# Optimization experiments

Hardware: AMD Instinct MI355X
Metric: run time of the kernel (lower is better)

The kernel has to match this reference:

```python
import jax, jax.numpy as jnp
import numpy as np

N_CLS = 5  # number of modalities / graph nodes


def _l2norm(x, eps=1e-12):
    n = jnp.linalg.norm(x, axis=-1, keepdims=True)
    return x / jnp.maximum(n, eps)


def _bn(x, g, b, eps=1e-5):
    """BatchNorm over channel axis 1 (training-mode batch stats), x: (B, Ch, ...)."""
    axes = (0,) + tuple(range(2, x.ndim))
    m = x.mean(axis=axes, keepdims=True)
    v = x.var(axis=axes, keepdims=True)
    shp = (1, -1) + (1,) * (x.ndim - 2)
    return g.reshape(shp) * (x - m) / jnp.sqrt(v + eps) + b.reshape(shp)


def _cross_attn(y, x, wq, wk, wv):
    """ME-GraphAU-style CrossAttn over the spatial (hw) axis. y,x: (..., hw, c)."""
    q = y @ wq  # (..., hw, c/2)
    k = x @ wk
    v = x @ wv
    scale = 1.0 / jnp.sqrt(jnp.asarray(wq.shape[1], jnp.float32))
    attn = jax.nn.softmax(jnp.einsum('...qd,...kd->...qk', q, k) * scale, axis=-1)
    return jnp.einsum('...qk,...kd->...qd', attn, v)


def _gnn_layer(x, edge, U, V, A, Bm, E, bnv_g, bnv_b, bne_g, bne_b, mask_node):
    """One edge-vertex GNN update. x: (b,n,t,c), edge: (b,n*n,t,c).
    Edge e = i*n + j has end-node i, start-node j (create_e_matrix layout)."""
    b, n, t, c = x.shape
    idx_i = jnp.repeat(jnp.arange(n), n)  # 'end' one-hot gather
    idx_j = jnp.tile(jnp.arange(n), n)    # 'start' one-hot gather
    res = x
    Vix = x @ A
    Vjx = x @ Bm
    e = edge @ E
    edge1 = Vix[:, idx_i] + Vjx[:, idx_j] + e  # einsum('ev,bvtc->betc') as gather
    edge1 = _bn(edge1, bne_g, bne_b)
    edge1 = jnp.where(jnp.isnan(edge1), 0.0, edge1)
    edge = edge + jax.nn.relu(edge1)
    eg = jax.nn.sigmoid(edge).reshape(b, n, n, t, c)
    eg = jax.nn.softmax(eg, axis=2).reshape(b, n * n, t, c)  # softmax over start nodes j
    Ujx = (x @ V)[:, idx_j]
    # einsum('ve,betc->bvtc', end.T, e*Ujx): scatter-sum edges to their end node i
    agg = (eg * Ujx).reshape(b, n, n, t, c).sum(axis=2) / n
    xn = x @ U + agg
    x1 = _bn(xn, bnv_g, bnv_b)
    if mask_node:
        x1 = jnp.where(jnp.isnan(x1), 0.0, x1)
    x = jax.nn.relu(res + x1)
    return x, edge


def _forward(af, ef, gf, attf, sf,
             fam_q, fam_k, fam_v, arm_q, arm_k, arm_v,
             edge_proj_w, edge_proj_b, gem_bn_g, gem_bn_b,
             U1, V1, A1, B1, E1, U2, V2, A2, B2, E2,
             bnv1_g, bnv1_b, bne1_g, bne1_b, bnv2_g, bnv2_b, bne2_g, bne2_b,
             sc, edge_fc_w, edge_fc_b):
    b, c, t, h, w = af.shape
    hw = h * w
    n = N_CLS

    def prep(f):  # (b,c,t,h,w) -> (b,t,hw,c)
        return f.reshape(b, c, t, hw).transpose(0, 2, 3, 1)

    mods = [prep(f) for f in (af, ef, gf, attf, sf)]
    f_u = jnp.stack(mods, axis=1)           # (b, 5, t, hw, c)
    f_v = f_u.mean(axis=-2)                 # (b, 5, t, c)

    # --- GEM edge extractor (ME-GraphAU style, adapted to the extra t axis) ---
    gfeat = jnp.broadcast_to(mods[0][:, None], f_u.shape)  # global feature = af
    feat = _cross_attn(f_u, gfeat, fam_q, fam_k, fam_v)    # FAM
    idx_i = jnp.repeat(jnp.arange(n), n)
    idx_j = jnp.tile(jnp.arange(n), n)
    feat_end = feat[:, idx_i]               # (b, 25, t, hw, c)
    feat_start = feat[:, idx_j]
    feat = _cross_attn(feat_start, feat_end, arm_q, arm_k, arm_v)  # ARM
    edge = feat @ edge_proj_w + edge_proj_b
    edge = _bn(edge.reshape(b, n * n, t * hw, c), gem_bn_g, gem_bn_b)
    f_e = edge.reshape(b, n * n, t, hw, c).mean(axis=-2)   # (b, 25, t, c)

    # --- 2-layer edge-vertex GNN ---
    f_v, f_e = _gnn_layer(f_v, f_e, U1, V1, A1, B1, E1,
                          bnv1_g, bnv1_b, bne1_g, bne1_b, mask_node=True)
    f_v, f_e = _gnn_layer(f_v, f_e, U2, V2, A2, B2, E2,
                          bnv2_g, bnv2_b, bne2_g, bne2_b, mask_node=False)

    # --- cosine-similarity head ---
    scn = _l2norm(jax.nn.relu(sc))                         # (5, c)
    cl = (_l2norm(f_v) * scn[None, :, None, :]).sum(axis=-1)  # (b, 5, t)
    cl_edge = jnp.einsum('bntc,c->bnt', f_e, edge_fc_w)[..., None] + edge_fc_b  # (b,25,t,1)
    return cl, cl_edge


def setup_inputs() -> dict:
    B, C, T, H, W = 8, 256, 16, 7, 7
    key = jax.random.key(0)
    ks = jax.random.split(key, 40)
    d = {}
    for i, name in enumerate(['af', 'ef', 'gf', 'attf', 'sf']):
        d[name] = jax.random.normal(ks[i], (B, C, T, H, W), jnp.float32)
    gs = float(np.sqrt(2.0 / C))   # GNN linear init scale
    xs = float(np.sqrt(2.0 / (2 * C)))  # xavier-like
    k = 5
    def nrm(shape, s):
        nonlocal k
        k += 1
        return jax.random.normal(ks[k], shape, jnp.float32) * s
    d['fam_q'] = nrm((C, C // 2), xs); d['fam_k'] = nrm((C, C // 2), xs); d['fam_v'] = nrm((C, C), xs)
    d['arm_q'] = nrm((C, C // 2), xs); d['arm_k'] = nrm((C, C // 2), xs); d['arm_v'] = nrm((C, C), xs)
    d['edge_proj_w'] = nrm((C, C), xs); d['edge_proj_b'] = jnp.zeros((C,), jnp.float32)
    d['gem_bn_g'] = jnp.ones((N_CLS * N_CLS,), jnp.float32); d['gem_bn_b'] = jnp.zeros((N_CLS * N_CLS,), jnp.float32)
    for nm in ['U1', 'V1', 'A1', 'B1', 'E1', 'U2', 'V2', 'A2', 'B2', 'E2']:
        d[nm] = nrm((C, C), gs)
    for nm, sz in [('bnv1', N_CLS), ('bne1', N_CLS * N_CLS), ('bnv2', N_CLS), ('bne2', N_CLS * N_CLS)]:
        d[nm + '_g'] = jnp.ones((sz,), jnp.float32)
        d[nm + '_b'] = jnp.zeros((sz,), jnp.float32)
    d['sc'] = nrm((N_CLS, C), xs)
    d['edge_fc_w'] = nrm((C,), xs)
    d['edge_fc_b'] = jnp.zeros((1,), jnp.float32)
    return d


def reference(af, ef, gf, attf, sf,
              fam_q, fam_k, fam_v, arm_q, arm_k, arm_v,
              edge_proj_w, edge_proj_b, gem_bn_g, gem_bn_b,
              U1, V1, A1, B1, E1, U2, V2, A2, B2, E2,
              bnv1_g, bnv1_b, bne1_g, bne1_b, bnv2_g, bnv2_b, bne2_g, bne2_b,
              sc, edge_fc_w, edge_fc_b):
    return _forward(af, ef, gf, attf, sf,
                    fam_q, fam_k, fam_v, arm_q, arm_k, arm_v,
                    edge_proj_w, edge_proj_b, gem_bn_g, gem_bn_b,
                    U1, V1, A1, B1, E1, U2, V2, A2, B2, E2,
                    bnv1_g, bnv1_b, bne1_g, bne1_b, bnv2_g, bnv2_b, bne2_g, bne2_b,
                    sc, edge_fc_w, edge_fc_b)
```

## Files before the change

### kernel.cpp

```cpp
#include <hip/hip_runtime.h>

#define DEV __device__ __forceinline__

typedef unsigned short bhalf;
typedef __attribute__((ext_vector_type(8))) short bf8v;
typedef __attribute__((ext_vector_type(4))) float f4;
typedef __attribute__((ext_vector_type(4))) unsigned short us4;

namespace {
constexpr int TPB = 256;
constexpr float ATT_SCALE = 0.08838834764831845f;

constexpr size_t O_PT  = 0;
constexpr size_t O_WTS = 20971520;
constexpr size_t O_K1B = 21626880;
constexpr size_t O_FW  = 23724032;
constexpr size_t O_VQT = 27918336;
constexpr size_t O_VKT = 30015488;
constexpr size_t O_G   = 32112640;
constexpr size_t O_VWT = 36306944;
constexpr size_t O_Q2B = 40501248;
constexpr size_t O_K2B = 50987008;
constexpr size_t O_W2T = 61472768;
constexpr size_t O_FV  = 82444288;
constexpr size_t O_HWS = 83099648;
constexpr size_t O_EDG = 86376448;
constexpr size_t O_XA  = 89654272;
constexpr size_t O_XB  = 90309632;
constexpr size_t O_XU  = 90964992;
constexpr size_t O_XV  = 91620352;
constexpr size_t O_EE  = 92275712;
constexpr size_t O_ET  = 95552512;
constexpr size_t O_XN  = 98829312;
constexpr size_t O_GWT = 99484672;
constexpr size_t O_CSE = 100795392;
constexpr size_t O_FVB = 100796416;
constexpr size_t O_HWB = 101124096;
constexpr size_t O_EDB = 102762496;

constexpr size_t W_FAMQ = 0, W_FAMK = 32768, W_ARMQ = 65536, W_ARMK = 98304,
                 W_FAMV = 131072, W_ARMV = 196608, W_EPW = 262144;
constexpr size_t FW_VQ = 0, FW_VK = 32768, FW_VW = 65536;

constexpr int ST_GS1 = 0, ST_GS2 = 256;
}


DEV bhalf f2b(float f) {
  unsigned u = __float_as_uint(f);
  return (bhalf)((u + 0x7FFFu + ((u >> 16) & 1u)) >> 16);
}

DEV f4 mfma16(bf8v a, bf8v b, f4 c) {
  return __builtin_amdgcn_mfma_f32_16x16x32_bf16(a, b, c, 0, 0, 0);
}

DEV bf8v ldfrag(const bhalf* base, int r0, int k0, int S, int l) {
  return *reinterpret_cast<const bf8v*>(base + (size_t)(r0 + (l & 15)) * S + k0 + ((l >> 4) << 3));
}

DEV bf8v ldswz(const bhalf* base, int row, int koffB, int strideB) {
  int byte = row * strideB + koffB;
  byte ^= ((row & 7) << 4);
  return *reinterpret_cast<const bf8v*>(reinterpret_cast<const char*>(base) + byte);
}

DEV float sumShards(const float* base, int idx) {
  float s = 0.f;
  #pragma unroll
  for (int x = 0; x < 8; ++x) s += base[x*32 + idx];
  return s;
}

DEV void regSoftmax(float sv[4][4]) {
  #pragma unroll
  for (int reg = 0; reg < 4; ++reg) {
    float m = fmaxf(fmaxf(sv[0][reg], sv[1][reg]), fmaxf(sv[2][reg], sv[3][reg]));
    #pragma unroll
    for (int off = 1; off <= 8; off <<= 1) m = fmaxf(m, __shfl_xor(m, off));
    float s = 0.f;
    #pragma unroll
    for (int nt = 0; nt < 4; ++nt) { float e = __expf(sv[nt][reg] - m); sv[nt][reg] = e; s += e; }
    #pragma unroll
    for (int off = 1; off <= 8; off <<= 1) s += __shfl_xor(s, off);
    float inv = 1.f / s;
    #pragma unroll
    for (int nt = 0; nt < 4; ++nt) sv[nt][reg] *= inv;
  }
}

DEV void reduce2Atomic(float a, float b, float* ga, float* gb, float* red) {
  #pragma unroll
  for (int off = 32; off; off >>= 1) { a += __shfl_down(a, off); b += __shfl_down(b, off); }
  if ((threadIdx.x & 63) == 0) { int w = threadIdx.x >> 6; red[w*2] = a; red[w*2+1] = b; }
  __syncthreads();
  if (threadIdx.x == 0) {
    atomicAdd(ga, red[0]+red[2]+red[4]+red[6]);
    atomicAdd(gb, red[1]+red[3]+red[5]+red[7]);
  }
  __syncthreads();
}


__global__ void __launch_bounds__(256) prepAll(const float* fq, const float* fk, const float* fv,
                                               const float* aq, const float* ak, const float* av,
                                               const float* ep, bhalf* WT,
                                               const float* af, const float* ef, const float* gf,
                                               const float* attf, const float* sf,
                                               bhalf* PT, float* FV, float* G,
                                               const float* A1, const float* B1, const float* U1,
                                               const float* V1, const float* E1,
                                               const float* A2, const float* B2, const float* U2,
                                               const float* V2, const float* E2,
                                               bhalf* GWT, float* CSE, bhalf* FVB) {
  __shared__ float lb[49*260];
  int tid = threadIdx.x;
  if (blockIdx.x < 1280) {
    int blk = blockIdx.x;
    const float* src; bhalf* dst; int N, n;
    if (blk < 512) {
      int m = blk >> 7; n = blk & 127; N = 128;
      src = (m==0)?fq:(m==1)?fk:(m==2)?aq:ak;
      dst = WT + (size_t)m*32768;
    } else {
      int r = blk - 512; int m = r >> 8; n = r & 255; N = 256;
      src = (m==0)?fv:(m==1)?av:ep;
      dst = WT + 131072 + (size_t)m*65536;
    }
    dst[(size_t)n*256 + tid] = f2b(src[(size_t)tid*N + n]);
  } else if (blockIdx.x < 1920) {
    int blk = blockIdx.x - 1280;
    int u = blk % 5, bt = blk / 5, b = bt >> 4, t = bt & 15;
    const float* src = (u==0)?af:(u==1)?ef:(u==2)?gf:(u==3)?attf:sf;
    src += ((size_t)b*256*16 + t)*49;
    for (int o = tid; o < 49*256; o += TPB) {
      int c = o / 49, p = o % 49;
      lb[p*260 + c] = src[(size_t)c*784 + p];
    }
    __syncthreads();
    bhalf* pt = PT + (size_t)blk*16384;
    for (int p = 0; p < 64; ++p)
      pt[p*256 + tid] = (p < 49) ? f2b(lb[p*260 + tid]) : (bhalf)0;
    float s = 0.f;
    for (int p = 0; p < 49; ++p) s += lb[p*260 + tid];
    float mval = s * (1.f/49.f);
    size_t idx = (((size_t)(b*5+u)*16) + t)*256 + tid;
    FV[idx] = mval;
    FVB[idx] = f2b(mval);
  } else if (blockIdx.x < 2176) {
    int c = blockIdx.x - 1920;
    const float* ar = av + (size_t)c*256;
    float acc = 0.f;
    for (int d = 0; d < 256; ++d)
      acc = fmaf(ar[d], ep[(size_t)d*256 + tid], acc);
    G[(size_t)c*256 + tid] = acc;
  } else if (blockIdx.x < 4736) {
    int blk = blockIdx.x - 2176;
    int m = blk >> 8, n = blk & 255;
    const float* src = (m==0)?A1:(m==1)?B1:(m==2)?U1:(m==3)?V1:(m==4)?E1:
                       (m==5)?A2:(m==6)?B2:(m==7)?U2:(m==8)?V2:E2;
    GWT[(size_t)m*65536 + (size_t)n*256 + tid] = f2b(src[(size_t)tid*256 + n]);
  } else {
    float s = 0.f;
    for (int c = 0; c < 256; ++c) s += E1[(size_t)c*256 + tid];
    CSE[tid] = s;
  }
}

__global__ void __launch_bounds__(256) wf2(const float* fv, const float* aq, const float* ak,
                                           const float* G, bhalf* FW) {
  int blk = blockIdx.x, tid = threadIdx.x;
  if (blk < 256) {
    int k = blk;
    if (tid < 128) {
      float a1 = 0.f, a2 = 0.f;
      for (int c = 0; c < 256; ++c) {
        float f = fv[(size_t)k*256 + c];
        a1 = fmaf(f, aq[(size_t)c*128 + tid], a1);
        a2 = fmaf(f, ak[(size_t)c*128 + tid], a2);
      }
      FW[FW_VQ + (size_t)tid*256 + k] = f2b(a1);
      FW[FW_VK + (size_t)tid*256 + k] = f2b(a2);
    }
  } else {
    int k = blk - 256;
    float a = 0.f;
    for (int c = 0; c < 256; ++c)
      a = fmaf(fv[(size_t)k*256 + c], G[(size_t)c*256 + tid], a);
    FW[FW_VW + (size_t)tid*256 + k] = f2b(a);
  }
}

__global__ void __launch_bounds__(256, 4) kv1(const bhalf* PT, const bhalf* WT, const bhalf* FW,
                                              bhalf* K1B, bhalf* VQT, bhalf* VKT, bhalf* VWT,
                                              bhalf* Q2B) {
  __shared__ bhalf Wl[64*256];
  int bt = blockIdx.x, part = blockIdx.y;
  int tid = threadIdx.x, w = tid >> 6, l = tid & 63;
  const bhalf* Wsrc; int nt0;
  const bhalf* A;
  if (part >= 10) {
    int u = (part - 10) >> 1;
    nt0 = ((part - 10) & 1) * 4;
    Wsrc = WT + W_FAMQ;
    A = PT + (size_t)(bt*5 + u)*16384;
  } else if (part < 2) {
    nt0 = part*4; Wsrc = WT + W_FAMK; A = PT + (size_t)bt*5*16384;
  } else if (part < 6) {
    nt0 = ((part - 2) & 1) * 4;
    Wsrc = FW + (((part - 2) >> 1) == 0 ? FW_VQ : FW_VK);
    A = PT + (size_t)bt*5*16384;
  } else {
    nt0 = (part - 6)*4; Wsrc = FW + FW_VW; A = PT + (size_t)bt*5*16384;
  }
  bf8v a8[8];
  #pragma unroll
  for (int kt = 0; kt < 8; ++kt) a8[kt] = ldfrag(A, w*16, kt*32, 256, l);
  {
    const char* gw = reinterpret_cast<const char*>(Wsrc + (size_t)nt0*16*256);
    char* lw = reinterpret_cast<char*>(Wl);
    #pragma unroll
    for (int c = 0; c < 8; ++c) {
      int x = (c*256 + tid) << 4;
      float4 val = *reinterpret_cast<const float4*>(gw + x);
      *reinterpret_cast<float4*>(lw + (x ^ (((x >> 9) & 7) << 4))) = val;
    }
  }
  __syncthreads();
  __builtin_amdgcn_s_setprio(1);
  f4 accs[4];
  #pragma unroll
  for (int nn = 0; nn < 4; ++nn) {
    f4 acc = {0.f,0.f,0.f,0.f};
    #pragma unroll
    for (int kt = 0; kt < 8; ++kt)
      acc = mfma16(a8[kt], ldswz(Wl, nn*16 + (l & 15), kt*64 + ((l >> 4) << 4), 512), acc);
    accs[nn] = acc;
  }
  __builtin_amdgcn_s_setprio(0);
  if (part >= 10) {
    int u = (part - 10) >> 1;
    bhalf* q1 = Q2B + (size_t)(bt*5 + u)*8192;
    #pragma unroll
    for (int nn = 0; nn < 4; ++nn) {
      int nt = nt0 + nn;
      #pragma unroll
      for (int reg = 0; reg < 4; ++reg) {
        int p = w*16 + ((l>>4)<<2) + reg;
        q1[(size_t)p*128 + nt*16 + (l&15)] = f2b(accs[nn][reg]);
      }
    }
  } else if (part < 2) {
    bhalf* dst = K1B + (size_t)bt*8192;
    #pragma unroll
    for (int nn = 0; nn < 4; ++nn) {
      int nt = nt0 + nn;
      #pragma unroll
      for (int reg = 0; reg < 4; ++reg) {
        int p = w*16 + ((l>>4)<<2) + reg;
        dst[(size_t)p*128 + nt*16 + (l&15)] = f2b(accs[nn][reg]);
      }
    }
  } else if (part < 6) {
    bhalf* o = ((((part - 2) >> 1) == 0) ? VQT : VKT) + (size_t)bt*8192;
    #pragma unroll
    for (int nn = 0; nn < 4; ++nn) {
      int n = (nt0 + nn)*16 + (l&15);
      int p0 = w*16 + ((l>>4)<<2);
      us4 pk = { f2b(accs[nn][0]), f2b(accs[nn][1]), f2b(accs[nn][2]), f2b(accs[nn][3]) };
      *reinterpret_cast<us4*>(o + (size_t)n*64 + p0) = pk;
    }
  } else {
    bhalf* ow = VWT + (size_t)bt*16384;
    #pragma unroll
    for (int nn = 0; nn < 4; ++nn) {
      int n = (nt0 + nn)*16 + (l&15);
      int p0 = w*16 + ((l>>4)<<2);
      us4 pk = { f2b(accs[nn][0]), f2b(accs[nn][1]), f2b(accs[nn][2]), f2b(accs[nn][3]) };
      *reinterpret_cast<us4*>(ow + (size_t)n*64 + p0) = pk;
    }
  }
}

__global__ void __launch_bounds__(256) s1ker(const bhalf* WT,
    const bhalf* K1B, const bhalf* VQT, const bhalf* VKT, const bhalf* VWT,
    bhalf* Q2B, bhalf* K2B, bhalf* W2T)
{
  __shared__ bhalf bufP[64*72];
  int orig = blockIdx.x;
  int blk = (orig & 7) * 80 + (orig >> 3);
  int bt = blk / 5;
  int tid = threadIdx.x, w = tid >> 6, l = tid & 63;
  float sv[4][4];
  {
    const bhalf* Q1 = Q2B + (size_t)blk*8192;
    const bhalf* K1 = K1B + (size_t)bt*8192;
    bf8v aq[4];
    #pragma unroll
    for (int kt = 0; kt < 4; ++kt) aq[kt] = ldfrag(Q1, w*16, kt*32, 128, l);
    __builtin_amdgcn_s_setprio(1);
    #pragma unroll
    for (int nt = 0; nt < 4; ++nt) {
      f4 acc = {0.f,0.f,0.f,0.f};
      #pragma unroll
      for (int kt = 0; kt < 4; ++kt)
        acc = mfma16(aq[kt], ldfrag(K1, nt*16, kt*32, 128, l), acc);
      #pragma unroll
      for (int reg = 0; reg < 4; ++reg) sv[nt][reg] = acc[reg] * ATT_SCALE;
    }
    __builtin_amdgcn_s_setprio(0);
  }
  if ((l & 15) > 0) { sv[3][0] = -1e30f; sv[3][1] = -1e30f; sv[3][2] = -1e30f; sv[3][3] = -1e30f; }
  regSoftmax(sv);
  #pragma unroll
  for (int nt = 0; nt < 4; ++nt)
    #pragma unroll
    for (int reg = 0; reg < 4; ++reg)
      bufP[(w*16 + ((l>>4)<<2) + reg)*72 + nt*16 + (l&15)] = f2b(sv[nt][reg]);
  __syncthreads();
  bf8v ap0[4], ap1[4];
  #pragma unroll
  for (int g = 0; g < 4; ++g) {
    ap0[g] = ldfrag(bufP, g*16, 0, 72, l);
    ap1[g] = ldfrag(bufP, g*16, 32, 72, l);
  }
  const bhalf* vq = VQT + (size_t)bt*8192;
  const bhalf* vk = VKT + (size_t)bt*8192;
  const bhalf* vw = VWT + (size_t)bt*16384;
  bhalf* q2 = Q2B + (size_t)blk*8192;
  bhalf* k2 = K2B + (size_t)blk*8192;
  bhalf* w2 = W2T + (size_t)blk*16384;
  __builtin_amdgcn_s_setprio(1);
  #pragma unroll
  for (int nn = 0; nn < 2; ++nn) {
    int nt = w*2 + nn;
    bf8v b0 = ldfrag(vq, nt*16, 0, 64, l);
    bf8v b1 = ldfrag(vq, nt*16, 32, 64, l);
    f4 acc[4];
    #pragma unroll
    for (int g = 0; g < 4; ++g) {
      f4 z = {0.f,0.f,0.f,0.f};
      z = mfma16(ap0[g], b0, z);
      acc[g] = mfma16(ap1[g], b1, z);
    }
    int c = nt*16 + (l & 15);
    #pragma unroll
    for (int g = 0; g < 4; ++g)
      #pragma unroll
      for (int reg = 0; reg < 4; ++reg) {
        int p = g*16 + ((l>>4)<<2) + reg;
        q2[(size_t)p*128 + c] = (p < 49) ? f2b(acc[g][reg]) : (bhalf)0;
      }
  }
  #pragma unroll
  for (int nn = 0; nn < 2; ++nn) {
    int nt = w*2 + nn;
    bf8v b0 = ldfrag(vk, nt*16, 0, 64, l);
    bf8v b1 = ldfrag(vk, nt*16, 32, 64, l);
    f4 acc[4];
    #pragma unroll
    for (int g = 0; g < 4; ++g) {
      f4 z = {0.f,0.f,0.f,0.f};
      z = mfma16(ap0[g], b0, z);
      acc[g] = mfma16(ap1[g], b1, z);
    }
    int c = nt*16 + (l & 15);
    #pragma unroll
    for (int g = 0; g < 4; ++g)
      #pragma unroll
      for (int reg = 0; reg < 4; ++reg) {
        int p = g*16 + ((l>>4)<<2) + reg;
        k2[(size_t)p*128 + c] = (p < 49) ? f2b(acc[g][reg]) : (bhalf)0;
      }
  }
  #pragma unroll
  for (int nn = 0; nn < 4; ++nn) {
    int nt = w*4 + nn;
    bf8v b0 = ldfrag(vw, nt*16, 0, 64, l);
    bf8v b1 = ldfrag(vw, nt*16, 32, 64, l);
    f4 acc[4];
    #pragma unroll
    for (int g = 0; g < 4; ++g) {
      f4 z = {0.f,0.f,0.f,0.f};
      z = mfma16(ap0[g], b0, z);
      acc[g] = mfma16(ap1[g], b1, z);
    }
    int c = nt*16 + (l & 15);
    int p0 = (l >> 4) << 2;
    #pragma unroll
    for (int g = 0; g < 4; ++g) {
      int pb = g*16 + p0;
      us4 pk = { (bhalf)((pb+0 < 49) ? f2b(acc[g][0]) : 0),
                 (bhalf)((pb+1 < 49) ? f2b(acc[g][1]) : 0),
                 (bhalf)((pb+2 < 49) ? f2b(acc[g][2]) : 0),
                 (bhalf)((pb+3 < 49) ? f2b(acc[g][3]) : 0) };
      *reinterpret_cast<us4*>(w2 + (size_t)c*64 + pb) = pk;
    }
  }
  __builtin_amdgcn_s_setprio(0);
}

__global__ void __launch_bounds__(256) s2ker(const bhalf* Q2B, const bhalf* K2B, const bhalf* W2T,
    const float* epb, float* hws, bhalf* hwsb, float* gs1, float* gs2)
{
  __shared__ bhalf Kl[64*128];
  __shared__ bhalf bufP[64*72];
  __shared__ float redH[256];
  __shared__ float redS[8];
  int orig = blockIdx.x;
  int blk = (orig & 7) * 400 + (orig >> 3);
  int e = blk % 25, bt = blk / 25, b = bt >> 4, t = bt & 15;
  int i = e / 5, j = e % 5;
  int tid = threadIdx.x, w = tid >> 6, l = tid & 63;
  const bhalf* K = K2B + (size_t)(bt*5 + i)*8192;
  const bhalf* V = W2T + (size_t)(bt*5 + i)*16384;
  const bhalf* Q = Q2B + (size_t)(bt*5 + j)*8192;
  bf8v aq[4];
  #pragma unroll
  for (int kt = 0; kt < 4; ++kt) aq[kt] = ldfrag(Q, w*16, kt*32, 128, l);
  {
    const char* gk = reinterpret_cast<const char*>(K);
    char* lk = reinterpret_cast<char*>(Kl);
    #pragma unroll
    for (int c = 0; c < 4; ++c) {
      int x = (c*256 + tid) << 4;
      float4 val = *reinterpret_cast<const float4*>(gk + x);
      *reinterpret_cast<float4*>(lk + (x ^ (((x >> 8) & 7) << 4))) = val;
    }
  }
  __syncthreads();
  float sv[4][4];
  __builtin_amdgcn_s_setprio(1);
  #pragma unroll
  for (int nt = 0; nt < 4; ++nt) {
    f4 acc = {0.f,0.f,0.f,0.f};
    #pragma unroll
    for (int kt = 0; kt < 4; ++kt)
      acc = mfma16(aq[kt], ldswz(Kl, nt*16 + (l & 15), kt*64 + ((l >> 4) << 4), 256), acc);
    #pragma unroll
    for (int reg = 0; reg < 4; ++reg) sv[nt][reg] = acc[reg] * ATT_SCALE;
  }
  __builtin_amdgcn_s_setprio(0);
  if ((l & 15) > 0) { sv[3][0] = -1e30f; sv[3][1] = -1e30f; sv[3][2] = -1e30f; sv[3][3] = -1e30f; }
  regSoftmax(sv);
  #pragma unroll
  for (int nt = 0; nt < 4; ++nt)
    #pragma unroll
    for (int reg = 0; reg < 4; ++reg)
      bufP[(w*16 + ((l>>4)<<2) + reg)*72 + nt*16 + (l&15)] = f2b(sv[nt][reg]);
  bf8v vf0[4], vf1[4];
  #pragma unroll
  for (int nn = 0; nn < 4; ++nn) {
    vf0[nn] = ldfrag(V, (w*4 + nn)*16, 0, 64, l);
    vf1[nn] = ldfrag(V, (w*4 + nn)*16, 32, 64, l);
  }
  __syncthreads();
  bf8v ap0[4], ap1[4];
  #pragma unroll
  for (int g = 0; g < 4; ++g) {
    ap0[g] = ldfrag(bufP, g*16, 0, 72, l);
    ap1[g] = ldfrag(bufP, g*16, 32, 72, l);
  }
  float sqa = 0.f;
  __builtin_amdgcn_s_setprio(1);
  #pragma unroll
  for (int nn = 0; nn < 4; ++nn) {
    f4 acc[4];
    #pragma unroll
    for (int g = 0; g < 4; ++g) {
      f4 z = {0.f,0.f,0.f,0.f};
      z = mfma16(ap0[g], vf0[nn], z);
      acc[g] = mfma16(ap1[g], vf1[nn], z);
    }
    int c = ((w*4 + nn) << 4) + (l & 15);
    float bias = epb[c];
    float hw = 0.f;
    #pragma unroll
    for (int g = 0; g < 4; ++g) {
      #pragma unroll
      for (int reg = 0; reg < 4; ++reg) {
        int p = g*16 + ((l>>4)<<2) + reg;
        if (p < 49) { float v = acc[g][reg] + bias; hw += v; sqa += v*v; }
      }
    }
    hw += __shfl_xor(hw, 16);
    hw += __shfl_xor(hw, 32);
    if ((l >> 4) == 0) redH[c] = hw;
  }
  __builtin_amdgcn_s_setprio(0);
  __syncthreads();
  float hwtot = redH[tid];
  size_t oidx = (((size_t)(b*25+e)*16) + t)*256 + tid;
  hws[oidx] = hwtot;
  hwsb[oidx] = f2b(hwtot);
  int slot = (orig & 7)*32 + e;
  reduce2Atomic(hwtot, sqa, gs1 + slot, gs2 + slot, redS);
}


__global__ void __launch_bounds__(256, 2) gnnProjN(const bhalf* Xb, const bhalf* GW,
    float* xA, float* xB, float* xU, float* xV) {
  __shared__ bhalf Wl[64*256];
  int blk = blockIdx.x;
  int tid = threadIdx.x, w = tid >> 6, l = tid & 63;
  int m = blk / 40, rem = blk % 40, rt = rem >> 2, ct = rem & 3;
  const bhalf* A = Xb + (size_t)rt*64*256;
  const bhalf* Wsrc = GW + (size_t)m*65536;
  float* dst = (m==0)?xA:(m==1)?xB:(m==2)?xU:xV;
  bf8v a8[8];
  #pragma unroll
  for (int kt = 0; kt < 8; ++kt) a8[kt] = ldfrag(A, w*16, kt*32, 256, l);
  {
    const char* gw = reinterpret_cast<const char*>(Wsrc + (size_t)ct*64*256);
    char* lw = reinterpret_cast<char*>(Wl);
    #pragma unroll
    for (int c = 0; c < 8; ++c) {
      int x = (c*256 + tid) << 4;
      float4 val = *reinterpret_cast<const float4*>(gw + x);
      *reinterpret_cast<float4*>(lw + (x ^ (((x >> 9) & 7) << 4))) = val;
    }
  }
  __syncthreads();
  __builtin_amdgcn_s_setprio(1);
  f4 accs[4];
  #pragma unroll
  for (int nn = 0; nn < 4; ++nn) {
    f4 acc = {0.f,0.f,0.f,0.f};
    #pragma unroll
    for (int kt = 0; kt < 8; ++kt)
      acc = mfma16(a8[kt], ldswz(Wl, nn*16 + (l & 15), kt*64 + ((l >> 4) << 4), 512), acc);
    accs[nn] = acc;
  }
  __builtin_amdgcn_s_setprio(0);
  int p0 = w*16 + ((l>>4)<<2);
  size_t rbase = (size_t)rt*64 + p0;
  #pragma unroll
  for (int nn = 0; nn < 4; ++nn) {
    int n = ct*64 + nn*16 + (l&15);
    #pragma unroll
    for (int reg = 0; reg < 4; ++reg)
      dst[(rbase + reg)*256 + n] = accs[nn][reg];
  }
}

__global__ void __launch_bounds__(256, 2) gnnProjE(const bhalf* Eb, const bhalf* GW,
    const float* CSE, const float* gs1, const float* gs2, const float* gg, const float* gb,
    int bnfly, const float* xA, const float* xB, float* ET, float* es1, float* es2) {
  __shared__ bhalf Wl[64*256];
  int blk = blockIdx.x;
  int tid = threadIdx.x, w = tid >> 6, l = tid & 63;
  int rt = blk >> 2, ct = blk & 3;
  const bhalf* A = Eb + (size_t)rt*64*256;
  bf8v a8[8];
  #pragma unroll
  for (int kt = 0; kt < 8; ++kt) a8[kt] = ldfrag(A, w*16, kt*32, 256, l);
  {
    const char* gw = reinterpret_cast<const char*>(GW + (size_t)ct*64*256);
    char* lw = reinterpret_cast<char*>(Wl);
    #pragma unroll
    for (int c = 0; c < 8; ++c) {
      int x = (c*256 + tid) << 4;
      float4 val = *reinterpret_cast<const float4*>(gw + x);
      *reinterpret_cast<float4*>(lw + (x ^ (((x >> 9) & 7) << 4))) = val;
    }
  }
  __syncthreads();
  __builtin_amdgcn_s_setprio(1);
  f4 accs[4];
  #pragma unroll
  for (int nn = 0; nn < 4; ++nn) {
    f4 acc = {0.f,0.f,0.f,0.f};
    #pragma unroll
    for (int kt = 0; kt < 8; ++kt)
      acc = mfma16(a8[kt], ldswz(Wl, nn*16 + (l & 15), kt*64 + ((l >> 4) << 4), 512), acc);
    accs[nn] = acc;
  }
  __builtin_amdgcn_s_setprio(0);
  int be = rt*4 + w;
  int b = be / 25, e = be % 25;
  int i = e / 5, j = e % 5;
  const float* xAr = xA + ((size_t)(b*5+i)*16)*256;
  const float* xBr = xB + ((size_t)(b*5+j)*16)*256;
  float scl = 1.f, ofs = 0.f;
  if (bnfly) {
    constexpr float invCnt = 1.f/1605632.f;
    float m = sumShards(gs1, e)*invCnt;
    float var = sumShards(gs2, e)*invCnt - m*m;
    float rstd = rsqrtf(var + 1e-5f);
    float g = gg[e]*rstd;
    scl = g * (1.f/49.f);
    ofs = gb[e] - g*m;
  }
  int t0 = (l>>4)<<2;
  float s1l = 0.f, s2l = 0.f;
  #pragma unroll
  for (int nn = 0; nn < 4; ++nn) {
    int n = ct*64 + nn*16 + (l&15);
    float cs = CSE[n] * ofs;
    #pragma unroll
    for (int reg = 0; reg < 4; ++reg) {
      int t = t0 + reg;
      float ve = fmaf(accs[nn][reg], scl, cs);
      float vfull = xAr[(size_t)t*256 + n] + xBr[(size_t)t*256 + n] + ve;
      ET[((size_t)be*16 + t)*256 + n] = vfull;
      s1l += vfull; s2l += vfull*vfull;
    }
  }
  #pragma unroll
  for (int off = 32; off; off >>= 1) { s1l += __shfl_down(s1l, off); s2l += __shfl_down(s2l, off); }
  if (l == 0) {
    int slot = (blk & 7)*32 + e;
    atomicAdd(es1 + slot, s1l);
    atomicAdd(es2 + slot, s2l);
  }
}

__global__ void __launch_bounds__(256) g2bg3a(const float* ET, const float* HWS, const float* EDGin,
    float* EDGout, bhalf* EDGb, const float* xV, const float* xU, float* XN,
    const float* gs1, const float* gs2, const float* gemg, const float* gemb,
    const float* bg, const float* bb2, const float* es1, const float* es2,
    float* ns1, float* ns2, const float* efw, const float* efb, float* out, int layer) {
  __shared__ float red[8];
  int blk = blockIdx.x, tid = threadIdx.x;
  int b = blk / 80, i = (blk >> 4) % 5, t = blk & 15;
  constexpr float inv32k = 1.f/32768.f;
  constexpr float invCnt = 1.f/1605632.f;
  float ssum = 0.f, exv[5], xvv[5];
  #pragma unroll
  for (int j = 0; j < 5; ++j) {
    int e = i*5 + j;
    size_t ee = ((size_t)(b*25 + e)*16 + t)*256 + tid;
    float m = sumShards(es1, e)*inv32k;
    float var = sumShards(es2, e)*inv32k - m*m;
    float rstd = rsqrtf(var + 1e-5f);
    float v = bg[e]*((ET[ee]-m)*rstd) + bb2[e];
    if (v != v) v = 0.f;
    float base;
    if (layer == 0) {
      float gm = sumShards(gs1, e)*invCnt;
      float gvar = sumShards(gs2, e)*invCnt - gm*gm;
      float gr = rsqrtf(gvar + 1e-5f);
      base = gemg[e]*((HWS[ee]*(1.f/49.f) - gm)*gr) + gemb[e];
    } else {
      base = EDGin[ee];
    }
    float edg = base + fmaxf(v, 0.f);
    if (layer == 0) {
      EDGout[ee] = edg;
      EDGb[ee] = f2b(edg);
    } else {
      float vv = edg * efw[tid];
      #pragma unroll
      for (int off = 32; off; off >>= 1) vv += __shfl_down(vv, off);
      if ((tid & 63) == 0) red[tid >> 6] = vv;
      __syncthreads();
      if (tid == 0) out[640 + (size_t)(b*25 + e)*16 + t] = red[0]+red[1]+red[2]+red[3] + efb[0];
      __syncthreads();
    }
    float sg = 1.f/(1.f + __expf(-edg));
    exv[j] = __expf(sg);
    ssum += exv[j];
    xvv[j] = xV[((size_t)(b*5+j)*16 + t)*256 + tid];
  }
  float agg = 0.f;
  #pragma unroll
  for (int j = 0; j < 5; ++j) agg += exv[j]*xvv[j];
  agg *= 0.2f/ssum;
  float xn = xU[(size_t)blk*256 + tid] + agg;
  XN[(size_t)blk*256 + tid] = xn;
  int slot = (blk & 7)*32 + i;
  reduce2Atomic(xn, xn*xn, ns1 + slot, ns2 + slot, red);
}

__global__ void __launch_bounds__(256) g3b(const float* XN, float* X, bhalf* Xb,
                                           const float* g, const float* bb,
                                           const float* s1, const float* s2, int mask) {
  int blk = blockIdx.x, tid = threadIdx.x;
  int i = (blk >> 4) % 5;
  size_t ni = (size_t)blk*256 + tid;
  constexpr float invCnt = 1.f/32768.f;
  float m = sumShards(s1, i)*invCnt;
  float var = sumShards(s2, i)*invCnt - m*m;
  float rstd = rsqrtf(var + 1e-5f);
  float v = g[i]*((XN[ni]-m)*rstd) + bb[i];
  if (mask && v != v) v = 0.f;
  float nv = fmaxf(X[ni] + v, 0.f);
  X[ni] = nv;
  Xb[ni] = f2b(nv);
}

__global__ void __launch_bounds__(256) g3bfin(const float* XN, const float* FV,
    const float* g, const float* bb, const float* s1, const float* s2,
    const float* sc, float* out) {
  __shared__ float red[12];
  int blk = blockIdx.x, tid = threadIdx.x;
  int i = (blk >> 4) % 5;
  size_t ni = (size_t)blk*256 + tid;
  constexpr float inv32k = 1.f/32768.f;
  float m = sumShards(s1, i)*inv32k;
  float var = sumShards(s2, i)*inv32k - m*m;
  float rstd = rsqrtf(var + 1e-5f);
  float v = g[i]*((XN[ni]-m)*rstd) + bb[i];
  float x = fmaxf(FV[ni] + v, 0.f);
  float s = fmaxf(sc[i*256 + tid], 0.f);
  float xx = x*x, ss = s*s, xs = x*s;
  #pragma unroll
  for (int off = 32; off; off >>= 1) {
    xx += __shfl_down(xx, off); ss += __shfl_down(ss, off); xs += __shfl_down(xs, off);
  }
  if ((tid & 63) == 0) { int w = tid >> 6; red[w*3] = xx; red[w*3+1] = ss; red[w*3+2] = xs; }
  __syncthreads();
  if (tid == 0) {
    float sxx = red[0]+red[3]+red[6]+red[9];
    float sss = red[1]+red[4]+red[7]+red[10];
    float sxs = red[2]+red[5]+red[8]+red[11];
    float nx = fmaxf(sqrtf(sxx), 1e-12f);
    float ns = fmaxf(sqrtf(sss), 1e-12f);
    out[blk] = sxs / (nx * ns);
  }
}


extern "C" void kernel_launch(void* const* d_in, const int* in_sizes, int n_in,
                              void* d_out, int out_size, void* d_ws, size_t ws_size,
                              hipStream_t stream) {
  (void)in_sizes; (void)n_in; (void)out_size; (void)ws_size;
  const float* af    = (const float*)d_in[0];
  const float* ef    = (const float*)d_in[1];
  const float* gfm   = (const float*)d_in[2];
  const float* attf  = (const float*)d_in[3];
  const float* sfm   = (const float*)d_in[4];
  const float* fam_q = (const float*)d_in[5];
  const float* fam_k = (const float*)d_in[6];
  const float* fam_v = (const float*)d_in[7];
  const float* arm_q = (const float*)d_in[8];
  const float* arm_k = (const float*)d_in[9];
  const float* arm_v = (const float*)d_in[10];
  const float* epw   = (const float*)d_in[11];
  const float* epb   = (const float*)d_in[12];
  const float* gemg  = (const float*)d_in[13];
  const float* gemb  = (const float*)d_in[14];
  const float* Us[2]   = {(const float*)d_in[15], (const float*)d_in[20]};
  const float* Vs[2]   = {(const float*)d_in[16], (const float*)d_in[21]};
  const float* As[2]   = {(const float*)d_in[17], (const float*)d_in[22]};
  const float* Bs[2]   = {(const float*)d_in[18], (const float*)d_in[23]};
  const float* Es[2]   = {(const float*)d_in[19], (const float*)d_in[24]};
  const float* bnvg[2] = {(const float*)d_in[25], (const float*)d_in[29]};
  const float* bnvb[2] = {(const float*)d_in[26], (const float*)d_in[30]};
  const float* bneg[2] = {(const float*)d_in[27], (const float*)d_in[31]};
  const float* bneb[2] = {(const float*)d_in[28], (const float*)d_in[32]};
  const float* scp  = (const float*)d_in[33];
  const float* efw  = (const float*)d_in[34];
  const float* efb  = (const float*)d_in[35];

  char* ws = (char*)d_ws;
  bhalf* PT  = (bhalf*)(ws + O_PT);
  bhalf* WTS = (bhalf*)(ws + O_WTS);
  bhalf* K1B = (bhalf*)(ws + O_K1B);
  bhalf* FW  = (bhalf*)(ws + O_FW);
  bhalf* VQT = (bhalf*)(ws + O_VQT);
  bhalf* VKT = (bhalf*)(ws + O_VKT);
  float* G   = (float*)(ws + O_G);
  float* ST2 = (float*)(ws + O_G);
  bhalf* VWT = (bhalf*)(ws + O_VWT);
  bhalf* Q2B = (bhalf*)(ws + O_Q2B);
  bhalf* K2B = (bhalf*)(ws + O_K2B);
  bhalf* W2T = (bhalf*)(ws + O_W2T);
  float* FV  = (float*)(ws + O_FV);
  float* HWS = (float*)(ws + O_HWS);
  float* EDG = (float*)(ws + O_EDG);
  float* XA  = (float*)(ws + O_XA);
  float* XB  = (float*)(ws + O_XB);
  float* XU  = (float*)(ws + O_XU);
  float* XV  = (float*)(ws + O_XV);
  float* ET  = (float*)(ws + O_ET);
  float* XN  = (float*)(ws + O_XN);
  bhalf* GWT = (bhalf*)(ws + O_GWT);
  float* CSE = (float*)(ws + O_CSE);
  bhalf* FVB = (bhalf*)(ws + O_FVB);
  bhalf* HWB = (bhalf*)(ws + O_HWB);
  bhalf* EDB = (bhalf*)(ws + O_EDB);

  prepAll<<<4737, TPB, 0, stream>>>(fam_q, fam_k, fam_v, arm_q, arm_k, arm_v, epw, WTS,
                                    af, ef, gfm, attf, sfm, PT, FV, G,
                                    As[0], Bs[0], Us[0], Vs[0], Es[0],
                                    As[1], Bs[1], Us[1], Vs[1], Es[1],
                                    GWT, CSE, FVB);
  wf2<<<512, TPB, 0, stream>>>(fam_v, arm_q, arm_k, G, FW);
  hipMemsetAsync(ST2, 0, 2560*sizeof(float), stream);
  kv1<<<dim3(128, 20), TPB, 0, stream>>>(PT, WTS, FW, K1B, VQT, VKT, VWT, Q2B);
  s1ker<<<640, TPB, 0, stream>>>(WTS, K1B, VQT, VKT, VWT, Q2B, K2B, W2T);
  s2ker<<<3200, TPB, 0, stream>>>(Q2B, K2B, W2T, epb, HWS, HWB, ST2 + ST_GS1, ST2 + ST_GS2);

  float* out = (float*)d_out;
  for (int L = 0; L < 2; ++L) {
    float* es1 = ST2 + 512 + L*1024;
    float* es2 = ST2 + 768 + L*1024;
    float* ns1 = ST2 + 1024 + L*1024;
    float* ns2 = ST2 + 1280 + L*1024;
    gnnProjN<<<160, TPB, 0, stream>>>(FVB, GWT + (size_t)L*5*65536, XA, XB, XU, XV);
    gnnProjE<<<200, TPB, 0, stream>>>((L == 0) ? HWB : EDB,
                                      GWT + (size_t)L*5*65536 + (size_t)4*65536, CSE,
                                      ST2 + ST_GS1, ST2 + ST_GS2, gemg, gemb, (L == 0) ? 1 : 0,
                                      XA, XB, ET, es1, es2);
    g2bg3a<<<640, TPB, 0, stream>>>(ET, HWS, EDG, EDG, EDB, XV, XU, XN,
                                    ST2 + ST_GS1, ST2 + ST_GS2, gemg, gemb,
                                    bneg[L], bneb[L], es1, es2, ns1, ns2,
                                    efw, efb, out, L);
    if (L == 0)
      g3b<<<640, TPB, 0, stream>>>(XN, FV, FVB, bnvg[0], bnvb[0], ns1, ns2, 1);
    else
      g3bfin<<<640, TPB, 0, stream>>>(XN, FV, bnvg[1], bnvb[1], ns1, ns2, scp, out);
  }
}
```

Before: 165.6 us.

## Fuse layer-0 node BN/ReLU into layer-1 projection and merge prep launches

Removes the g3b kernel by recomputing layer-0 node batchnorm, residual and ReLU inside a new gnnProjNL1 prologue, with g3bfin repeating the same recompute for the final output. Moves the VQ/VK half of wf2 and the stats memset into prepAll, and gives the stats buffer its own workspace region instead of aliasing G. This cuts kernel launches and a full write/read of the intermediate node features, at the cost of redundant BN recomputation and reading fp32 inputs in the projection.

```diff
diff --git a/kernel.cpp b/kernel.cpp
--- a/kernel.cpp
+++ b/kernel.cpp
@@ -37,6 +37,7 @@
 constexpr size_t O_FVB = 100796416;
 constexpr size_t O_HWB = 101124096;
 constexpr size_t O_EDB = 102762496;
+constexpr size_t O_ST2 = 104400896;
 
 constexpr size_t W_FAMQ = 0, W_FAMK = 32768, W_ARMQ = 65536, W_ARMK = 98304,
                  W_FAMV = 131072, W_ARMV = 196608, W_EPW = 262144;
@@ -112,7 +113,8 @@
                                                const float* V1, const float* E1,
                                                const float* A2, const float* B2, const float* U2,
                                                const float* V2, const float* E2,
-                                               bhalf* GWT, float* CSE, bhalf* FVB) {
+                                               bhalf* GWT, float* CSE, bhalf* FVB,
+                                               bhalf* FW, float* ST2) {
   __shared__ float lb[49*260];
   int tid = threadIdx.x;
   if (blockIdx.x < 1280) {
@@ -160,18 +162,13 @@
     const float* src = (m==0)?A1:(m==1)?B1:(m==2)?U1:(m==3)?V1:(m==4)?E1:
                        (m==5)?A2:(m==6)?B2:(m==7)?U2:(m==8)?V2:E2;
     GWT[(size_t)m*65536 + (size_t)n*256 + tid] = f2b(src[(size_t)tid*256 + n]);
-  } else {
+  } else if (blockIdx.x == 4736) {
     float s = 0.f;
     for (int c = 0; c < 256; ++c) s += E1[(size_t)c*256 + tid];
     CSE[tid] = s;
-  }
-}
-
-__global__ void __launch_bounds__(256) wf2(const float* fv, const float* aq, const float* ak,
-                                           const float* G, bhalf* FW) {
-  int blk = blockIdx.x, tid = threadIdx.x;
-  if (blk < 256) {
-    int k = blk;
+    for (int o = tid; o < 2560; o += TPB) ST2[o] = 0.f;
+  } else {
+    int k = blockIdx.x - 4737;
     if (tid < 128) {
       float a1 = 0.f, a2 = 0.f;
       for (int c = 0; c < 256; ++c) {
@@ -182,13 +179,15 @@
       FW[FW_VQ + (size_t)tid*256 + k] = f2b(a1);
       FW[FW_VK + (size_t)tid*256 + k] = f2b(a2);
     }
-  } else {
-    int k = blk - 256;
-    float a = 0.f;
-    for (int c = 0; c < 256; ++c)
-      a = fmaf(fv[(size_t)k*256 + c], G[(size_t)c*256 + tid], a);
-    FW[FW_VW + (size_t)tid*256 + k] = f2b(a);
-  }
+  }
+}
+
+__global__ void __launch_bounds__(256) wf2(const float* fv, const float* G, bhalf* FW) {
+  int k = blockIdx.x, tid = threadIdx.x;
+  float a = 0.f;
+  for (int c = 0; c < 256; ++c)
+    a = fmaf(fv[(size_t)k*256 + c], G[(size_t)c*256 + tid], a);
+  FW[FW_VW + (size_t)tid*256 + k] = f2b(a);
 }
 
 __global__ void __launch_bounds__(256, 4) kv1(const bhalf* PT, const bhalf* WT, const bhalf* FW,
@@ -543,6 +542,72 @@
   }
 }
 
+__global__ void __launch_bounds__(256, 2) gnnProjNL1(const float* FVold, const float* XN0,
+    const bhalf* GW, const float* g0, const float* b0, const float* ns1, const float* ns2,
+    float* xA, float* xB, float* xU, float* xV) {
+  __shared__ bhalf Wl[64*256];
+  int blk = blockIdx.x;
+  int tid = threadIdx.x, w = tid >> 6, l = tid & 63;
+  int m = blk / 40, rem = blk % 40, rt = rem >> 2, ct = rem & 3;
+  const bhalf* Wsrc = GW + (size_t)m*65536;
+  float* dst = (m==0)?xA:(m==1)?xB:(m==2)?xU:xV;
+  int i = (rt*4 + w) % 5;
+  constexpr float inv32k = 1.f/32768.f;
+  float m0 = sumShards(ns1, i)*inv32k;
+  float var0 = sumShards(ns2, i)*inv32k - m0*m0;
+  float r0 = rsqrtf(var0 + 1e-5f);
+  float gi = g0[i], bi = b0[i];
+  int row = rt*64 + w*16 + (l & 15);
+  bf8v a8[8];
+  #pragma unroll
+  for (int kt = 0; kt < 8; ++kt) {
+    size_t base = (size_t)row*256 + kt*32 + ((l >> 4) << 3);
+    float4 fa = *reinterpret_cast<const float4*>(&FVold[base]);
+    float4 fb = *reinterpret_cast<const float4*>(&FVold[base + 4]);
+    float4 xa = *reinterpret_cast<const float4*>(&XN0[base]);
+    float4 xb = *reinterpret_cast<const float4*>(&XN0[base + 4]);
+    float xv[8] = {xa.x, xa.y, xa.z, xa.w, xb.x, xb.y, xb.z, xb.w};
+    float fv[8] = {fa.x, fa.y, fa.z, fa.w, fb.x, fb.y, fb.z, fb.w};
+    #pragma unroll
+    for (int q = 0; q < 8; ++q) {
+      float v = gi*((xv[q] - m0)*r0) + bi;
+      if (v != v) v = 0.f;
+      a8[kt][q] = (short)f2b(fmaxf(fv[q] + v, 0.f));
+    }
+  }
+  {
+    const char* gw = reinterpret_cast<const char*>(Wsrc + (size_t)ct*64*256);
+    char* lw = reinterpret_cast<char*>(Wl);
+    #pragma unroll
+    for (int c = 0; c < 8; ++c) {
+      int x = (c*256 + tid) << 4;
+      float4 val = *reinterpret_cast<const float4*>(gw + x);
+      *reinterpret_cast<float4*>(lw + (x ^ (((x >> 9) & 7) << 4))) = val;
+    }
+  }
+  __syncthreads();
+  __builtin_amdgcn_s_setprio(1);
+  f4 accs[4];
+  #pragma unroll
+  for (int nn = 0; nn < 4; ++nn) {
+    f4 acc = {0.f,0.f,0.f,0.f};
+    #pragma unroll
+    for (int kt = 0; kt < 8; ++kt)
+      acc = mfma16(a8[kt], ldswz(Wl, nn*16 + (l & 15), kt*64 + ((l >> 4) << 4), 512), acc);
+    accs[nn] = acc;
+  }
+  __builtin_amdgcn_s_setprio(0);
+  int p0 = w*16 + ((l>>4)<<2);
+  size_t rbase = (size_t)rt*64 + p0;
+  #pragma unroll
+  for (int nn = 0; nn < 4; ++nn) {
+    int n = ct*64 + nn*16 + (l&15);
+    #pragma unroll
+    for (int reg = 0; reg < 4; ++reg)
+      dst[(rbase + reg)*256 + n] = accs[nn][reg];
+  }
+}
+
 __global__ void __launch_bounds__(256, 2) gnnProjE(const bhalf* Eb, const bhalf* GW,
     const float* CSE, const float* gs1, const float* gs2, const float* gg, const float* gb,
     int bnfly, const float* xA, const float* xB, float* ET, float* es1, float* es2) {
@@ -672,36 +737,26 @@
   reduce2Atomic(xn, xn*xn, ns1 + slot, ns2 + slot, red);
 }
 
-__global__ void __launch_bounds__(256) g3b(const float* XN, float* X, bhalf* Xb,
-                                           const float* g, const float* bb,
-                                           const float* s1, const float* s2, int mask) {
-  int blk = blockIdx.x, tid = threadIdx.x;
-  int i = (blk >> 4) % 5;
-  size_t ni = (size_t)blk*256 + tid;
-  constexpr float invCnt = 1.f/32768.f;
-  float m = sumShards(s1, i)*invCnt;
-  float var = sumShards(s2, i)*invCnt - m*m;
-  float rstd = rsqrtf(var + 1e-5f);
-  float v = g[i]*((XN[ni]-m)*rstd) + bb[i];
-  if (mask && v != v) v = 0.f;
-  float nv = fmaxf(X[ni] + v, 0.f);
-  X[ni] = nv;
-  Xb[ni] = f2b(nv);
-}
-
-__global__ void __launch_bounds__(256) g3bfin(const float* XN, const float* FV,
-    const float* g, const float* bb, const float* s1, const float* s2,
+__global__ void __launch_bounds__(256) g3bfin(const float* XN1, const float* XN0, const float* FVold,
+    const float* g1v, const float* b1v, const float* s1_1, const float* s2_1,
+    const float* g0v, const float* b0v, const float* s1_0, const float* s2_0,
     const float* sc, float* out) {
   __shared__ float red[12];
   int blk = blockIdx.x, tid = threadIdx.x;
   int i = (blk >> 4) % 5;
   size_t ni = (size_t)blk*256 + tid;
   constexpr float inv32k = 1.f/32768.f;
-  float m = sumShards(s1, i)*inv32k;
-  float var = sumShards(s2, i)*inv32k - m*m;
-  float rstd = rsqrtf(var + 1e-5f);
-  float v = g[i]*((XN[ni]-m)*rstd) + bb[i];
-  float x = fmaxf(FV[ni] + v, 0.f);
+  float m0 = sumShards(s1_0, i)*inv32k;
+  float var0 = sumShards(s2_0, i)*inv32k - m0*m0;
+  float rstd0 = rsqrtf(var0 + 1e-5f);
+  float v0 = g0v[i]*((XN0[ni]-m0)*rstd0) + b0v[i];
+  if (v0 != v0) v0 = 0.f;
+  float fvnew = fmaxf(FVold[ni] + v0, 0.f);
+  float m1 = sumShards(s1_1, i)*inv32k;
+  float var1 = sumShards(s2_1, i)*inv32k - m1*m1;
+  float rstd1 = rsqrtf(var1 + 1e-5f);
+  float v1 = g1v[i]*((XN1[ni]-m1)*rstd1) + b1v[i];
+  float x = fmaxf(fvnew + v1, 0.f);
   float s = fmaxf(sc[i*256 + tid], 0.f);
   float xx = x*x, ss = s*s, xs = x*s;
   #pragma unroll
@@ -761,7 +816,6 @@
   bhalf* VQT = (bhalf*)(ws + O_VQT);
   bhalf* VKT = (bhalf*)(ws + O_VKT);
   float* G   = (float*)(ws + O_G);
-  float* ST2 = (float*)(ws + O_G);
   bhalf* VWT = (bhalf*)(ws + O_VWT);
   bhalf* Q2B = (bhalf*)(ws + O_Q2B);
   bhalf* K2B = (bhalf*)(ws + O_K2B);
@@ -774,42 +828,53 @@
   float* XU  = (float*)(ws + O_XU);
   float* XV  = (float*)(ws + O_XV);
   float* ET  = (float*)(ws + O_ET);
-  float* XN  = (float*)(ws + O_XN);
+  float* XN0 = (float*)(ws + O_XN);
+  float* XN1 = (float*)(ws + O_EE);
   bhalf* GWT = (bhalf*)(ws + O_GWT);
   float* CSE = (float*)(ws + O_CSE);
   bhalf* FVB = (bhalf*)(ws + O_FVB);
   bhalf* HWB = (bhalf*)(ws + O_HWB);
   bhalf* EDB = (bhalf*)(ws + O_EDB);
-
-  prepAll<<<4737, TPB, 0, stream>>>(fam_q, fam_k, fam_v, arm_q, arm_k, arm_v, epw, WTS,
+  float* ST2 = (float*)(ws + O_ST2);
+
+  prepAll<<<4993, TPB, 0, stream>>>(fam_q, fam_k, fam_v, arm_q, arm_k, arm_v, epw, WTS,
                                     af, ef, gfm, attf, sfm, PT, FV, G,
                                     As[0], Bs[0], Us[0], Vs[0], Es[0],
                                     As[1], Bs[1], Us[1], Vs[1], Es[1],
-                                    GWT, CSE, FVB);
-  wf2<<<512, TPB, 0, stream>>>(fam_v, arm_q, arm_k, G, FW);
-  hipMemsetAsync(ST2, 0, 2560*sizeof(float), stream);
+                                    GWT, CSE, FVB, FW, ST2);
+  wf2<<<256, TPB, 0, stream>>>(fam_v, G, FW);
   kv1<<<dim3(128, 20), TPB, 0, stream>>>(PT, WTS, FW, K1B, VQT, VKT, VWT, Q2B);
   s1ker<<<640, TPB, 0, stream>>>(WTS, K1B, VQT, VKT, VWT, Q2B, K2B, W2T);
   s2ker<<<3200, TPB, 0, stream>>>(Q2B, K2B, W2T, epb, HWS, HWB, ST2 + ST_GS1, ST2 + ST_GS2);
 
   float* out = (float*)d_out;
+  float* es1_0 = ST2 + 512;          float* es2_0 = ST2 + 768;
+  float* ns1_0 = ST2 + 1024;         float* ns2_0 = ST2 + 1280;
+  float* es1_1 = ST2 + 512 + 1024;   float* es2_1 = ST2 + 768 + 1024;
+  float* ns1_1 = ST2 + 1024 + 1024;  float* ns2_1 = ST2 + 1280 + 1024;
+
   for (int L = 0; L < 2; ++L) {
-    float* es1 = ST2 + 512 + L*1024;
-    float* es2 = ST2 + 768 + L*1024;
-    float* ns1 = ST2 + 1024 + L*1024;
-    float* ns2 = ST2 + 1280 + L*1024;
-    gnnProjN<<<160, TPB, 0, stream>>>(FVB, GWT + (size_t)L*5*65536, XA, XB, XU, XV);
+    float* es1 = (L == 0) ? es1_0 : es1_1;
+    float* es2 = (L == 0) ? es2_0 : es2_1;
+    float* ns1 = (L == 0) ? ns1_0 : ns1_1;
+    float* ns2 = (L == 0) ? ns2_0 : ns2_1;
+    if (L == 0)
+      gnnProjN<<<160, TPB, 0, stream>>>(FVB, GWT, XA, XB, XU, XV);
+    else
+      gnnProjNL1<<<160, TPB, 0, stream>>>(FV, XN0, GWT + (size_t)5*65536,
+                                          bnvg[0], bnvb[0], ns1_0, ns2_0,
+                                          XA, XB, XU, XV);
     gnnProjE<<<200, TPB, 0, stream>>>((L == 0) ? HWB : EDB,
                                       GWT + (size_t)L*5*65536 + (size_t)4*65536, CSE,
                                       ST2 + ST_GS1, ST2 + ST_GS2, gemg, gemb, (L == 0) ? 1 : 0,
                                       XA, XB, ET, es1, es2);
-    g2bg3a<<<640, TPB, 0, stream>>>(ET, HWS, EDG, EDG, EDB, XV, XU, XN,
+    g2bg3a<<<640, TPB, 0, stream>>>(ET, HWS, EDG, EDG, EDB, XV, XU, (L == 0) ? XN0 : XN1,
                                     ST2 + ST_GS1, ST2 + ST_GS2, gemg, gemb,
                                     bneg[L], bneb[L], es1, es2, ns1, ns2,
                                     efw, efb, out, L);
-    if (L == 0)
-      g3b<<<640, TPB, 0, stream>>>(XN, FV, FVB, bnvg[0], bnvb[0], ns1, ns2, 1);
-    else
-      g3bfin<<<640, TPB, 0, stream>>>(XN, FV, bnvg[1], bnvb[1], ns1, ns2, scp, out);
-  }
-}
+  }
+  g3bfin<<<640, TPB, 0, stream>>>(XN1, XN0, FV,
+                                  bnvg[1], bnvb[1], ns1_1, ns2_1,
+                                  bnvg[0], bnvb[0], ns1_0, ns2_0,
+                                  scp, out);
+}
```

After: 168.2 us. No clear change (+1.5%).
